# Optimization experiments

Hardware: AMD Instinct MI355X
Metric: run time of the kernel (lower is better)

The kernel has to match this reference:

```python
import jax, jax.numpy as jnp
import numpy as np

EMBED_DIM = 1024
NUM_HEADS = 16
HEAD_DIM = EMBED_DIM // NUM_HEADS


def setup_inputs() -> dict:
    key = jax.random.key(0)
    k_x, k_wq, k_bq, k_wo, k_bo = jax.random.split(key, 5)
    B, S, E = 4, 2048, EMBED_DIM
    lim_qkv = 1.0 / np.sqrt(E)
    lim_out = 1.0 / np.sqrt(E)
    return {
        "x": jax.random.normal(k_x, (B, S, E), dtype=jnp.float32),
        # nn.Linear stores weight [out, in]; we keep [in, out] for x @ W
        "w_qkv": jax.random.uniform(k_wq, (E, 3 * E), minval=-lim_qkv, maxval=lim_qkv, dtype=jnp.float32),
        "b_qkv": jax.random.uniform(k_bq, (3 * E,), minval=-lim_qkv, maxval=lim_qkv, dtype=jnp.float32),
        "w_out": jax.random.uniform(k_wo, (E, E), minval=-lim_out, maxval=lim_out, dtype=jnp.float32),
        "b_out": jax.random.uniform(k_bo, (E,), minval=-lim_out, maxval=lim_out, dtype=jnp.float32),
    }


def reference(x, w_qkv, b_qkv, w_out, b_out):
    B, S, E = x.shape
    H, D = NUM_HEADS, HEAD_DIM
    qkv = x @ w_qkv + b_qkv                       # [B, S, 3E]
    qkv = qkv.reshape(B, S, H, 3 * D)
    q, k, v = jnp.split(qkv, 3, axis=-1)          # each [B, S, H, D]
    scale = 1.0 / np.sqrt(D).astype(np.float32)
    scores = jnp.einsum("bshd,bthd->bhst", q, k) * scale  # [B, H, S, S]
    attn = jax.nn.softmax(scores, axis=-1)
    out = jnp.einsum("bhst,bthd->bshd", attn, v)  # [B, S, H, D]
    out = out.reshape(B, S, E)
    return out @ w_out + b_out
```

## Files before the change

kernel.cpp:

```cpp
#include <hip/hip_runtime.h>
#include <hip/hip_bf16.h>


typedef short bf16x8 __attribute__((ext_vector_type(8)));
typedef unsigned short u16x8 __attribute__((ext_vector_type(8)));
typedef short s16x4 __attribute__((ext_vector_type(4)));
typedef float f32x4 __attribute__((ext_vector_type(4)));

#define QSCALE 0.18033688011112042f

__device__ inline short f2bf(float f) {
    unsigned int u = __builtin_bit_cast(unsigned int, f);
    u += 0x7fffu + ((u >> 16) & 1u);
    return (short)(u >> 16);
}

__device__ inline unsigned int pack2bf(float a, float b) {
#if __has_builtin(__builtin_amdgcn_cvt_pk_bf16_f32)
    typedef __bf16 bf2 __attribute__((ext_vector_type(2)));
    bf2 v = __builtin_amdgcn_cvt_pk_bf16_f32(a, b);
    return __builtin_bit_cast(unsigned int, v);
#else
    return (unsigned int)(unsigned short)f2bf(a) |
           ((unsigned int)(unsigned short)f2bf(b) << 16);
#endif
}

__device__ inline float fast_exp2(float x) {
#if __has_builtin(__builtin_amdgcn_exp2f)
    return __builtin_amdgcn_exp2f(x);
#else
    float r;
    asm("v_exp_f32 %0, %1" : "=v"(r) : "v"(x));
    return r;
#endif
}

__device__ inline float fast_rcp(float x) {
#if __has_builtin(__builtin_amdgcn_rcpf)
    return __builtin_amdgcn_rcpf(x);
#else
    float r;
    asm("v_rcp_f32 %0, %1" : "=v"(r) : "v"(x));
    return r;
#endif
}

__device__ inline void gload_lds16(const short* g, short* l) {
    __builtin_amdgcn_global_load_lds(
        (const __attribute__((address_space(1))) unsigned int*)g,
        (__attribute__((address_space(3))) unsigned int*)l, 16, 0, 0);
}

__global__ __launch_bounds__(256) void prep_kernel(
        const float* __restrict__ x, short* __restrict__ xb,
        const float* __restrict__ w_qkv, short* __restrict__ wqkvT,
        const float* __restrict__ w_out, short* __restrict__ woutT) {
    const int bid = blockIdx.x;
    if (bid < 4096) {
        int i = bid * 256 + threadIdx.x;
        const float4 a = *(const float4*)(x + (size_t)i * 8);
        const float4 b = *(const float4*)(x + (size_t)i * 8 + 4);
        uint4 o = {pack2bf(a.x, a.y), pack2bf(a.z, a.w),
                   pack2bf(b.x, b.y), pack2bf(b.z, b.w)};
        *(uint4*)(xb + (size_t)i * 8) = o;
        return;
    }
    __shared__ float tile[32][33];
    const float* in; short* out; int N, bx, by;
    if (bid < 7168) { int k = bid - 4096; bx = k % 96; by = k / 96; in = w_qkv; out = wqkvT; N = 3072; }
    else            { int k = bid - 7168; bx = k & 31; by = k >> 5; in = w_out; out = woutT; N = 1024; }
    const int K = 1024;
    int tx = threadIdx.x & 31, ty = threadIdx.x >> 5;
    int nt = bx * 32, kt = by * 32;
    for (int i = 0; i < 4; ++i)
        tile[ty + i * 8][tx] = in[(size_t)(kt + ty + i * 8) * N + nt + tx];
    __syncthreads();
    for (int i = 0; i < 4; ++i)
        out[(size_t)(nt + ty + i * 8) * K + kt + tx] = f2bf(tile[tx][ty + i * 8]);
}

__global__ __launch_bounds__(256, 2) void gemm_qkv_kernel(
        const short* __restrict__ A, const short* __restrict__ Bt,
        const float* __restrict__ bias,
        short* __restrict__ Qg, short* __restrict__ Kg, short* __restrict__ Vtg) {
    __shared__ short As[128 * 64];
    __shared__ short Bs[128 * 64];
    const int t = threadIdx.x;
    const int w = t >> 6, lane = t & 63, r = lane & 15, q4 = lane >> 4;
    const int n0 = blockIdx.x * 128, m0 = blockIdx.y * 128;
    const int wm = (w & 1) * 64, wn = (w >> 1) * 64;

    f32x4 acc[4][4];
    for (int i = 0; i < 4; ++i)
        for (int j = 0; j < 4; ++j)
            acc[i][j] = (f32x4){0.f, 0.f, 0.f, 0.f};

    for (int kk = 0; kk < 1024; kk += 64) {
        for (int ii = 0; ii < 4; ++ii) {
            const int p = t + 256 * ii;
            const int row = p >> 3;
            const int gg = (p & 7) ^ (row & 7);
            gload_lds16(A + (size_t)(m0 + row) * 1024 + kk + gg * 8, &As[p * 8]);
            gload_lds16(Bt + (size_t)(n0 + row) * 1024 + kk + gg * 8, &Bs[p * 8]);
        }
        __syncthreads();
        for (int ko = 0; ko < 2; ++ko) {
            bf16x8 af[4], bfr[4];
            for (int i = 0; i < 4; ++i) {
                const int R = wm + i * 16 + r;
                af[i] = *(const bf16x8*)(&As[R * 64 + (((ko * 4 + q4) ^ (R & 7)) * 8)]);
            }
            for (int j = 0; j < 4; ++j) {
                const int R = wn + j * 16 + r;
                bfr[j] = *(const bf16x8*)(&Bs[R * 64 + (((ko * 4 + q4) ^ (R & 7)) * 8)]);
            }
            for (int i = 0; i < 4; ++i)
                for (int j = 0; j < 4; ++j)
                    acc[i][j] = __builtin_amdgcn_mfma_f32_16x16x32_bf16(bfr[j], af[i], acc[i][j], 0, 0, 0);
        }
        __syncthreads();
    }

    for (int i = 0; i < 4; ++i) {
        const int gm = m0 + wm + i * 16 + r;
        const int bb = gm >> 11;
        const int s2 = gm & 2047;
        for (int j = 0; j < 4; ++j) {
            const int gnb = n0 + wn + j * 16 + q4 * 4;
            const int h = gnb / 192;
            const int rr = gnb - h * 192;
            const float4 bv = *(const float4*)(bias + gnb);
            const float v0 = acc[i][j][0] + bv.x;
            const float v1 = acc[i][j][1] + bv.y;
            const float v2 = acc[i][j][2] + bv.z;
            const float v3 = acc[i][j][3] + bv.w;
            const size_t bh = (size_t)(bb * 16 + h);
            if (rr < 64) {
                uint2 p = {pack2bf(v0 * QSCALE, v1 * QSCALE),
                           pack2bf(v2 * QSCALE, v3 * QSCALE)};
                *(uint2*)(Qg + (bh * 2048 + s2) * 64 + rr) = p;
            } else if (rr < 128) {
                uint2 p = {pack2bf(v0, v1), pack2bf(v2, v3)};
                *(uint2*)(Kg + (bh * 2048 + s2) * 64 + (rr - 64)) = p;
            } else {
                const int d0 = rr - 128;
                Vtg[(bh * 64 + d0 + 0) * 2048 + s2] = f2bf(v0);
                Vtg[(bh * 64 + d0 + 1) * 2048 + s2] = f2bf(v1);
                Vtg[(bh * 64 + d0 + 2) * 2048 + s2] = f2bf(v2);
                Vtg[(bh * 64 + d0 + 3) * 2048 + s2] = f2bf(v3);
            }
        }
    }
}

__global__ __launch_bounds__(256, 4) void attn_kernel(
        const short* __restrict__ Qg, const short* __restrict__ Kg,
        const short* __restrict__ Vtg, short* __restrict__ Og) {
    __shared__ short Ks[2][64 * 64];
    __shared__ short Vs[2][64 * 64];
    __shared__ short Ps[4 * 16 * 64];
    const int t = threadIdx.x;
    const int w = t >> 6, lane = t & 63, r = lane & 15, q4 = lane >> 4;
    const int blk0 = blockIdx.x;
    const int blk = ((blk0 & 7) << 7) | (blk0 >> 3);
    const int qt = blk & 15;
    const int h = (blk >> 4) & 15;
    const int b = blk >> 8;
    const size_t bh = (size_t)b * 16 + h;
    const short* Qb = Qg + bh * 2048 * 64;
    const short* Kb = Kg + bh * 2048 * 64;
    const short* Vb = Vtg + bh * 64 * 2048;

    const int r1 = t >> 3, g1 = (t & 7) ^ (r1 & 7);
    const int r2 = 32 + (t >> 3), g2 = (t & 7) ^ (r2 & 7);
    const short* kptr1 = Kb + r1 * 64 + g1 * 8;
    const short* kptr2 = Kb + r2 * 64 + g2 * 8;
    const short* vptr1 = Vb + (size_t)r1 * 2048 + g1 * 8;
    const short* vptr2 = Vb + (size_t)r2 * 2048 + g2 * 8;

    const int swz = r & 7;
    const int ga = (q4 ^ swz) * 8;
    const int gb = ((4 + q4) ^ swz) * 8;

    bf16x8 qf[2][2];
    for (int qs = 0; qs < 2; ++qs) {
        const int qrow = qt * 128 + w * 32 + qs * 16 + r;
        qf[qs][0] = *(const bf16x8*)(Qb + (size_t)qrow * 64 + q4 * 8);
        qf[qs][1] = *(const bf16x8*)(Qb + (size_t)qrow * 64 + 32 + q4 * 8);
    }

    bf16x8 onesf;
    for (int i = 0; i < 8; ++i) onesf[i] = (short)0x3F80;

    f32x4 o[2][4], ol[2];
    for (int qs = 0; qs < 2; ++qs) {
        ol[qs] = (f32x4){0.f, 0.f, 0.f, 0.f};
        for (int nt = 0; nt < 4; ++nt) o[qs][nt] = (f32x4){0.f, 0.f, 0.f, 0.f};
    }

    const int pbase0 = w * 1024;
    const int pwb = pbase0 + r * 64 + (q4 & 1) * 4;
    const int pgq = q4 >> 1;
    const int prb = pbase0 + r * 64;

    gload_lds16(kptr1, &Ks[0][t * 8]);
    gload_lds16(kptr2, &Ks[0][(256 + t) * 8]);
    gload_lds16(vptr1, &Vs[0][t * 8]);
    gload_lds16(vptr2, &Vs[0][(256 + t) * 8]);
    __syncthreads();

    int buf = 0;
    for (int kt = 0; kt < 32; ++kt) {
        const int nb = buf ^ 1;

        if (kt + 1 < 32) {
            gload_lds16(kptr1 + (kt + 1) * 4096, &Ks[nb][t * 8]);
            gload_lds16(kptr2 + (kt + 1) * 4096, &Ks[nb][(256 + t) * 8]);
            gload_lds16(vptr1 + (kt + 1) * 64, &Vs[nb][t * 8]);
            gload_lds16(vptr2 + (kt + 1) * 64, &Vs[nb][(256 + t) * 8]);
        }

        const short* Kl = Ks[buf];
        f32x4 st[2][4];
        __builtin_amdgcn_s_setprio(1);
#pragma unroll
        for (int c = 0; c < 4; ++c) {
            const int R = (c * 16 + r) * 64;
            const bf16x8 kf0 = *(const bf16x8*)(&Kl[R + ga]);
            const bf16x8 kf1 = *(const bf16x8*)(&Kl[R + gb]);
#pragma unroll
            for (int qs = 0; qs < 2; ++qs) {
                f32x4 z = (f32x4){0.f, 0.f, 0.f, 0.f};
                z = __builtin_amdgcn_mfma_f32_16x16x32_bf16(kf0, qf[qs][0], z, 0, 0, 0);
                z = __builtin_amdgcn_mfma_f32_16x16x32_bf16(kf1, qf[qs][1], z, 0, 0, 0);
                st[qs][c] = z;
            }
        }
        __builtin_amdgcn_s_setprio(0);

        unsigned int pk[2][4][2];
#pragma unroll
        for (int qs = 0; qs < 2; ++qs)
#pragma unroll
            for (int c = 0; c < 4; ++c) {
                const float p0 = fast_exp2(st[qs][c][0]);
                const float p1 = fast_exp2(st[qs][c][1]);
                const float p2 = fast_exp2(st[qs][c][2]);
                const float p3 = fast_exp2(st[qs][c][3]);
                pk[qs][c][0] = pack2bf(p0, p1);
                pk[qs][c][1] = pack2bf(p2, p3);
            }

#pragma unroll
        for (int c = 0; c < 4; ++c) {
            uint2 u = {pk[0][c][0], pk[0][c][1]};
            *(uint2*)(&Ps[pwb + (((c * 2 + pgq) ^ swz) * 8)]) = u;
        }
        bf16x8 pf0[2];
        pf0[0] = *(const bf16x8*)(&Ps[prb + ((q4 ^ swz) * 8)]);
        pf0[1] = *(const bf16x8*)(&Ps[prb + (((4 + q4) ^ swz) * 8)]);
#pragma unroll
        for (int c = 0; c < 4; ++c) {
            uint2 u = {pk[1][c][0], pk[1][c][1]};
            *(uint2*)(&Ps[pwb + (((c * 2 + pgq) ^ swz) * 8)]) = u;
        }
        bf16x8 pf1[2];
        pf1[0] = *(const bf16x8*)(&Ps[prb + ((q4 ^ swz) * 8)]);
        pf1[1] = *(const bf16x8*)(&Ps[prb + (((4 + q4) ^ swz) * 8)]);
        asm volatile("s_waitcnt lgkmcnt(0)" ::: "memory");

        const short* Vl = Vs[buf];
        __builtin_amdgcn_s_setprio(1);
#pragma unroll
        for (int ko = 0; ko < 2; ++ko) {
            const int gk = (ko == 0) ? ga : gb;
            const bf16x8 pfa = (ko == 0) ? pf0[0] : pf0[1];
            const bf16x8 pfb = (ko == 0) ? pf1[0] : pf1[1];
            ol[0] = __builtin_amdgcn_mfma_f32_16x16x32_bf16(onesf, pfa, ol[0], 0, 0, 0);
            ol[1] = __builtin_amdgcn_mfma_f32_16x16x32_bf16(onesf, pfb, ol[1], 0, 0, 0);
#pragma unroll
            for (int nt = 0; nt < 4; ++nt) {
                const bf16x8 vf = *(const bf16x8*)(&Vl[(nt * 16 + r) * 64 + gk]);
                o[0][nt] = __builtin_amdgcn_mfma_f32_16x16x32_bf16(vf, pfa, o[0][nt], 0, 0, 0);
                o[1][nt] = __builtin_amdgcn_mfma_f32_16x16x32_bf16(vf, pfb, o[1][nt], 0, 0, 0);
            }
        }
        __builtin_amdgcn_s_setprio(0);

        __syncthreads();
        buf = nb;
    }

    for (int qs = 0; qs < 2; ++qs) {
        const float inv = fast_rcp(ol[qs][0]);
        const int srow = qt * 128 + w * 32 + qs * 16 + r;
        const size_t base = ((size_t)(b * 2048 + srow)) * 1024 + h * 64;
        for (int nt = 0; nt < 4; ++nt) {
            uint2 pko = {pack2bf(o[qs][nt][0] * inv, o[qs][nt][1] * inv),
                         pack2bf(o[qs][nt][2] * inv, o[qs][nt][3] * inv)};
            *(uint2*)(Og + base + nt * 16 + q4 * 4) = pko;
        }
    }
}

__global__ __launch_bounds__(256, 2) void gemm_out_kernel(
        const short* __restrict__ A, const short* __restrict__ Bt,
        const float* __restrict__ bias, float* __restrict__ out) {
    __shared__ short As[128 * 64];
    __shared__ short Bs[128 * 64];
    const int t = threadIdx.x;
    const int w = t >> 6, lane = t & 63, r = lane & 15, q4 = lane >> 4;
    const int n0 = blockIdx.x * 128, m0 = blockIdx.y * 128;
    const int wm = (w & 1) * 64, wn = (w >> 1) * 64;

    f32x4 acc[4][4];
    for (int i = 0; i < 4; ++i)
        for (int j = 0; j < 4; ++j)
            acc[i][j] = (f32x4){0.f, 0.f, 0.f, 0.f};

    for (int kk = 0; kk < 1024; kk += 64) {
        for (int ii = 0; ii < 4; ++ii) {
            const int p = t + 256 * ii;
            const int row = p >> 3;
            const int gg = (p & 7) ^ (row & 7);
            gload_lds16(A + (size_t)(m0 + row) * 1024 + kk + gg * 8, &As[p * 8]);
            gload_lds16(Bt + (size_t)(n0 + row) * 1024 + kk + gg * 8, &Bs[p * 8]);
        }
        __syncthreads();
        for (int ko = 0; ko < 2; ++ko) {
            bf16x8 af[4], bfr[4];
            for (int i = 0; i < 4; ++i) {
                const int R = wm + i * 16 + r;
                af[i] = *(const bf16x8*)(&As[R * 64 + (((ko * 4 + q4) ^ (R & 7)) * 8)]);
            }
            for (int j = 0; j < 4; ++j) {
                const int R = wn + j * 16 + r;
                bfr[j] = *(const bf16x8*)(&Bs[R * 64 + (((ko * 4 + q4) ^ (R & 7)) * 8)]);
            }
            for (int i = 0; i < 4; ++i)
                for (int j = 0; j < 4; ++j)
                    acc[i][j] = __builtin_amdgcn_mfma_f32_16x16x32_bf16(bfr[j], af[i], acc[i][j], 0, 0, 0);
        }
        __syncthreads();
    }

    for (int i = 0; i < 4; ++i) {
        const int gm = m0 + wm + i * 16 + r;
        for (int j = 0; j < 4; ++j) {
            const int gnb = n0 + wn + j * 16 + q4 * 4;
            const float4 bv = *(const float4*)(bias + gnb);
            float4 v = {acc[i][j][0] + bv.x, acc[i][j][1] + bv.y,
                        acc[i][j][2] + bv.z, acc[i][j][3] + bv.w};
            *(float4*)(out + (size_t)gm * 1024 + gnb) = v;
        }
    }
}


extern "C" void kernel_launch(void* const* d_in, const int* in_sizes, int n_in,
                              void* d_out, int out_size, void* d_ws, size_t ws_size,
                              hipStream_t stream) {
    const float* x     = (const float*)d_in[0];
    const float* w_qkv = (const float*)d_in[1];
    const float* b_qkv = (const float*)d_in[2];
    const float* w_out = (const float*)d_in[3];
    const float* b_out = (const float*)d_in[4];
    float* out = (float*)d_out;

    char* ws = (char*)d_ws;
    short* xb    = (short*)(ws);
    short* wqkvT = (short*)(ws + 16777216);
    short* woutT = (short*)(ws + 23068672);
    short* Qg    = (short*)(ws + 25165824);
    short* Kg    = (short*)(ws + 41943040);
    short* Vtg   = (short*)(ws + 58720256);
    short* attn  = xb;

    prep_kernel<<<8192, 256, 0, stream>>>(x, xb, w_qkv, wqkvT, w_out, woutT);
    gemm_qkv_kernel<<<dim3(24, 64), 256, 0, stream>>>(xb, wqkvT, b_qkv, Qg, Kg, Vtg);
    attn_kernel<<<1024, 256, 0, stream>>>(Qg, Kg, Vtg, attn);
    gemm_out_kernel<<<dim3(8, 64), 256, 0, stream>>>(attn, woutT, b_out, out);
}
```

Before: 282.1 us.

## Rewrite projection GEMMs as 256x256 double-buffered 8-wave pipelined kernels

Both projection GEMMs move from 128x128 tiles with 4 waves and a single LDS buffer to 256x256 tiles with 8 waves. LDS is double-buffered and global loads are staged in quarter-tile pieces interleaved with MFMA phases, using explicit vmcnt waits, raw barriers and priority hints. Block IDs are remapped so neighbouring blocks share operand tiles in cache. The aim is to hide global-load latency and raise data reuse per block. The trade-off is fewer blocks: the output GEMM launches only 128 blocks, which may underfill the GPU. The hand-written waitcnt choreography is also fragile.

Measured after the change: 347.9 us. +23.3%, slower.

```diff
diff --git a/kernel.cpp b/kernel.cpp
--- a/kernel.cpp
+++ b/kernel.cpp
@@ -80,49 +80,130 @@
         out[(size_t)(nt + ty + i * 8) * K + kt + tx] = f2bf(tile[tx][ty + i * 8]);
 }
 
-__global__ __launch_bounds__(256, 2) void gemm_qkv_kernel(
-        const short* __restrict__ A, const short* __restrict__ Bt,
+#define G8_STAGE_A(slot_, h_, kt_) do {                                          \
+    _Pragma("unroll")                                                            \
+    for (int ii = 0; ii < 2; ++ii) {                                             \
+        const int p_ = t + 512 * ii;                                             \
+        const int row_ = p_ >> 3;                                                \
+        const int g_ = (p_ & 7) ^ (row_ & 7);                                    \
+        const int gm_ = m0 + (row_ & 63) + (h_) * 64 + (row_ >> 6) * 128;        \
+        gload_lds16(Agl + (size_t)gm_ * 1024 + (kt_) * 64 + g_ * 8,              \
+                    &As[slot_][(h_) * 8192 + p_ * 8]);                           \
+    } } while (0)
+
+#define G8_STAGE_B(slot_, h_, kt_) do {                                          \
+    _Pragma("unroll")                                                            \
+    for (int ii = 0; ii < 2; ++ii) {                                             \
+        const int p_ = t + 512 * ii;                                             \
+        const int row_ = p_ >> 3;                                                \
+        const int g_ = (p_ & 7) ^ (row_ & 7);                                    \
+        const int gn_ = n0 + (row_ & 31) + (h_) * 32 + (row_ >> 5) * 64;         \
+        gload_lds16(Btgl + (size_t)gn_ * 1024 + (kt_) * 64 + g_ * 8,             \
+                    &Bs[slot_][(h_) * 8192 + p_ * 8]);                           \
+    } } while (0)
+
+#define G8_READ_A(slot_, mh_) do {                                               \
+    _Pragma("unroll")                                                            \
+    for (int i2 = 0; i2 < 4; ++i2) {                                             \
+        const int row_ = i2 * 16 + r + rowa_off;                                 \
+        _Pragma("unroll")                                                        \
+        for (int ko = 0; ko < 2; ++ko)                                           \
+            af[i2][ko] = *(const bf16x8*)(&As[slot_][(mh_) * 8192 + row_ * 64 +  \
+                                          (((ko * 4 + q4) ^ (row_ & 7)) * 8)]);  \
+    } } while (0)
+
+#define G8_READ_B(slot_, nh_) do {                                               \
+    _Pragma("unroll")                                                            \
+    for (int j2 = 0; j2 < 2; ++j2) {                                             \
+        const int row_ = j2 * 16 + r + rowb_off;                                 \
+        _Pragma("unroll")                                                        \
+        for (int ko = 0; ko < 2; ++ko)                                           \
+            bfr[j2][ko] = *(const bf16x8*)(&Bs[slot_][(nh_) * 8192 + row_ * 64 + \
+                                           (((ko * 4 + q4) ^ (row_ & 7)) * 8)]); \
+    } } while (0)
+
+#define G8_MFMA(mh_, nh_) do {                                                   \
+    __builtin_amdgcn_s_setprio(1);                                               \
+    _Pragma("unroll")                                                            \
+    for (int i2 = 0; i2 < 4; ++i2)                                               \
+        _Pragma("unroll")                                                        \
+        for (int j2 = 0; j2 < 2; ++j2)                                           \
+            _Pragma("unroll")                                                    \
+            for (int ko = 0; ko < 2; ++ko)                                       \
+                acc[(mh_) * 4 + i2][(nh_) * 2 + j2] =                            \
+                    __builtin_amdgcn_mfma_f32_16x16x32_bf16(                     \
+                        bfr[j2][ko], af[i2][ko],                                 \
+                        acc[(mh_) * 4 + i2][(nh_) * 2 + j2], 0, 0, 0);           \
+    __builtin_amdgcn_s_setprio(0);                                               \
+} while (0)
+
+#define G8_BAR()  __builtin_amdgcn_s_barrier()
+#define G8_LGKM0() asm volatile("s_waitcnt lgkmcnt(0)" ::: "memory")
+
+#define G8_MAINLOOP()                                                            \
+    G8_STAGE_A(0, 0, 0); G8_STAGE_B(0, 0, 0); G8_STAGE_B(0, 1, 0); G8_STAGE_A(0, 1, 0); \
+    asm volatile("s_waitcnt vmcnt(4)" ::: "memory");                             \
+    G8_BAR();                                                                    \
+    _Pragma("unroll 1")                                                          \
+    for (int u = 0; u < 16; ++u) {                                               \
+        const int s = u & 1, ns = s ^ 1;                                         \
+                                     \
+        G8_READ_A(s, 0); G8_READ_B(s, 0);                                        \
+        if (u < 15) G8_STAGE_A(ns, 0, u + 1);                                    \
+        G8_BAR(); G8_LGKM0();                                                    \
+        G8_MFMA(0, 0);                                                           \
+        if (u < 15) { asm volatile("s_waitcnt vmcnt(4)" ::: "memory"); }         \
+        else        { asm volatile("s_waitcnt vmcnt(2)" ::: "memory"); }         \
+        G8_BAR();                                                                \
+                                                            \
+        G8_READ_B(s, 1);                                                         \
+        if (u < 15) G8_STAGE_B(ns, 0, u + 1);                                    \
+        G8_BAR(); G8_LGKM0();                                                    \
+        G8_MFMA(0, 1);                                                           \
+        if (u < 15) { asm volatile("s_waitcnt vmcnt(4)" ::: "memory"); }         \
+        else        { asm volatile("s_waitcnt vmcnt(0)" ::: "memory"); }         \
+        G8_BAR();                                                                \
+                                                            \
+        G8_READ_A(s, 1);                                                         \
+        if (u < 15) G8_STAGE_B(ns, 1, u + 1);                                    \
+        G8_BAR(); G8_LGKM0();                                                    \
+        G8_MFMA(1, 1);                                                           \
+        G8_BAR();                                                                \
+                                                            \
+        G8_READ_B(s, 0);                                                         \
+        if (u < 15) G8_STAGE_A(ns, 1, u + 1);                                    \
+        G8_BAR(); G8_LGKM0();                                                    \
+        G8_MFMA(1, 0);                                                           \
+        if (u < 15) { asm volatile("s_waitcnt vmcnt(4)" ::: "memory"); }         \
+        G8_BAR();                                                                \
+    }
+
+__global__ __launch_bounds__(512, 1) void gemm_qkv_kernel(
+        const short* __restrict__ Agl, const short* __restrict__ Btgl,
         const float* __restrict__ bias,
         short* __restrict__ Qg, short* __restrict__ Kg, short* __restrict__ Vtg) {
-    __shared__ short As[128 * 64];
-    __shared__ short Bs[128 * 64];
+    __shared__ __align__(16) short As[2][256 * 64];
+    __shared__ __align__(16) short Bs[2][256 * 64];
     const int t = threadIdx.x;
     const int w = t >> 6, lane = t & 63, r = lane & 15, q4 = lane >> 4;
-    const int n0 = blockIdx.x * 128, m0 = blockIdx.y * 128;
-    const int wm = (w & 1) * 64, wn = (w >> 1) * 64;
-
-    f32x4 acc[4][4];
-    for (int i = 0; i < 4; ++i)
+    const int wm = (w >> 2) * 128, wn = (w & 3) * 64;
+    const int rowa_off = (w >> 2) * 64, rowb_off = (w & 3) * 32;
+    const int fid = blockIdx.x;
+    const int blk = (fid & 7) * 48 + (fid >> 3);
+    const int bx = blk >> 5, by = blk & 31;
+    const int n0 = bx * 256, m0 = by * 256;
+
+    f32x4 acc[8][4];
+#pragma unroll
+    for (int i = 0; i < 8; ++i)
+#pragma unroll
         for (int j = 0; j < 4; ++j)
             acc[i][j] = (f32x4){0.f, 0.f, 0.f, 0.f};
-
-    for (int kk = 0; kk < 1024; kk += 64) {
-        for (int ii = 0; ii < 4; ++ii) {
-            const int p = t + 256 * ii;
-            const int row = p >> 3;
-            const int gg = (p & 7) ^ (row & 7);
-            gload_lds16(A + (size_t)(m0 + row) * 1024 + kk + gg * 8, &As[p * 8]);
-            gload_lds16(Bt + (size_t)(n0 + row) * 1024 + kk + gg * 8, &Bs[p * 8]);
-        }
-        __syncthreads();
-        for (int ko = 0; ko < 2; ++ko) {
-            bf16x8 af[4], bfr[4];
-            for (int i = 0; i < 4; ++i) {
-                const int R = wm + i * 16 + r;
-                af[i] = *(const bf16x8*)(&As[R * 64 + (((ko * 4 + q4) ^ (R & 7)) * 8)]);
-            }
-            for (int j = 0; j < 4; ++j) {
-                const int R = wn + j * 16 + r;
-                bfr[j] = *(const bf16x8*)(&Bs[R * 64 + (((ko * 4 + q4) ^ (R & 7)) * 8)]);
-            }
-            for (int i = 0; i < 4; ++i)
-                for (int j = 0; j < 4; ++j)
-                    acc[i][j] = __builtin_amdgcn_mfma_f32_16x16x32_bf16(bfr[j], af[i], acc[i][j], 0, 0, 0);
-        }
-        __syncthreads();
-    }
-
-    for (int i = 0; i < 4; ++i) {
+    bf16x8 af[4][2], bfr[2][2];
+
+    G8_MAINLOOP()
+
+    for (int i = 0; i < 8; ++i) {
         const int gm = m0 + wm + i * 16 + r;
         const int bb = gm >> 11;
         const int s2 = gm & 2047;
@@ -304,48 +385,31 @@
     }
 }
 
-__global__ __launch_bounds__(256, 2) void gemm_out_kernel(
-        const short* __restrict__ A, const short* __restrict__ Bt,
+__global__ __launch_bounds__(512, 1) void gemm_out_kernel(
+        const short* __restrict__ Agl, const short* __restrict__ Btgl,
         const float* __restrict__ bias, float* __restrict__ out) {
-    __shared__ short As[128 * 64];
-    __shared__ short Bs[128 * 64];
+    __shared__ __align__(16) short As[2][256 * 64];
+    __shared__ __align__(16) short Bs[2][256 * 64];
     const int t = threadIdx.x;
     const int w = t >> 6, lane = t & 63, r = lane & 15, q4 = lane >> 4;
-    const int n0 = blockIdx.x * 128, m0 = blockIdx.y * 128;
-    const int wm = (w & 1) * 64, wn = (w >> 1) * 64;
-
-    f32x4 acc[4][4];
-    for (int i = 0; i < 4; ++i)
+    const int wm = (w >> 2) * 128, wn = (w & 3) * 64;
+    const int rowa_off = (w >> 2) * 64, rowb_off = (w & 3) * 32;
+    const int fid = blockIdx.x;
+    const int blk = (fid & 7) * 16 + (fid >> 3);
+    const int bx = blk >> 5, by = blk & 31;
+    const int n0 = bx * 256, m0 = by * 256;
+
+    f32x4 acc[8][4];
+#pragma unroll
+    for (int i = 0; i < 8; ++i)
+#pragma unroll
         for (int j = 0; j < 4; ++j)
             acc[i][j] = (f32x4){0.f, 0.f, 0.f, 0.f};
-
-    for (int kk = 0; kk < 1024; kk += 64) {
-        for (int ii = 0; ii < 4; ++ii) {
-            const int p = t + 256 * ii;
-            const int row = p >> 3;
-            const int gg = (p & 7) ^ (row & 7);
-            gload_lds16(A + (size_t)(m0 + row) * 1024 + kk + gg * 8, &As[p * 8]);
-            gload_lds16(Bt + (size_t)(n0 + row) * 1024 + kk + gg * 8, &Bs[p * 8]);
-        }
-        __syncthreads();
-        for (int ko = 0; ko < 2; ++ko) {
-            bf16x8 af[4], bfr[4];
-            for (int i = 0; i < 4; ++i) {
-                const int R = wm + i * 16 + r;
-                af[i] = *(const bf16x8*)(&As[R * 64 + (((ko * 4 + q4) ^ (R & 7)) * 8)]);
-            }
-            for (int j = 0; j < 4; ++j) {
-                const int R = wn + j * 16 + r;
-                bfr[j] = *(const bf16x8*)(&Bs[R * 64 + (((ko * 4 + q4) ^ (R & 7)) * 8)]);
-            }
-            for (int i = 0; i < 4; ++i)
-                for (int j = 0; j < 4; ++j)
-                    acc[i][j] = __builtin_amdgcn_mfma_f32_16x16x32_bf16(bfr[j], af[i], acc[i][j], 0, 0, 0);
-        }
-        __syncthreads();
-    }
-
-    for (int i = 0; i < 4; ++i) {
+    bf16x8 af[4][2], bfr[2][2];
+
+    G8_MAINLOOP()
+
+    for (int i = 0; i < 8; ++i) {
         const int gm = m0 + wm + i * 16 + r;
         for (int j = 0; j < 4; ++j) {
             const int gnb = n0 + wn + j * 16 + q4 * 4;
@@ -378,7 +442,7 @@
     short* attn  = xb;
 
     prep_kernel<<<8192, 256, 0, stream>>>(x, xb, w_qkv, wqkvT, w_out, woutT);
-    gemm_qkv_kernel<<<dim3(24, 64), 256, 0, stream>>>(xb, wqkvT, b_qkv, Qg, Kg, Vtg);
+    gemm_qkv_kernel<<<384, 512, 0, stream>>>(xb, wqkvT, b_qkv, Qg, Kg, Vtg);
     attn_kernel<<<1024, 256, 0, stream>>>(Qg, Kg, Vtg, attn);
-    gemm_out_kernel<<<dim3(8, 64), 256, 0, stream>>>(attn, woutT, b_out, out);
-}
+    gemm_out_kernel<<<128, 512, 0, stream>>>(attn, woutT, b_out, out);
+}
```
